# Performance work log

Measured on AMD Instinct MI355X. Metric: run time of the kernel, lower is better.

Reference implementation:

```python
import jax, jax.numpy as jnp
import numpy as np

B, S, D, H = 4, 2048, 768, 12
HD = D // H  # head_dim = 64


def setup_inputs() -> dict:
    key = jax.random.key(0)
    ks = jax.random.split(key, 5)
    scale = 0.02
    return {
        "x": jax.random.normal(ks[0], (B, S, D), dtype=jnp.float32),
        "wq": jax.random.normal(ks[1], (D, D), dtype=jnp.float32) * scale,
        "wk": jax.random.normal(ks[2], (D, D), dtype=jnp.float32) * scale,
        "wv": jax.random.normal(ks[3], (D, D), dtype=jnp.float32) * scale,
        "wo": jax.random.normal(ks[4], (D, D), dtype=jnp.float32) * scale,
        "bo": jnp.zeros((D,), dtype=jnp.float32),
    }


def reference(x, wq, wk, wv, wo, bo):
    b, s, d = x.shape
    # torch Linear: y = x @ W.T ; qkv_bias=False
    q = (x @ wq.T).reshape(b, s, H, HD).transpose(0, 2, 1, 3)  # [b,h,s,hd]
    k = (x @ wk.T).reshape(b, s, H, HD).transpose(0, 2, 1, 3)
    v = (x @ wv.T).reshape(b, s, H, HD).transpose(0, 2, 1, 3)
    scores = jnp.einsum("bhqd,bhkd->bhqk", q, k)  # full [b,h,s,s] score matrix
    causal = jnp.triu(jnp.ones((s, s), dtype=bool), k=1)
    scores = jnp.where(causal, -jnp.inf, scores)
    attn = jax.nn.softmax(scores / jnp.sqrt(jnp.float32(HD)), axis=-1)
    ctx = jnp.einsum("bhqk,bhkd->bhqd", attn, v)
    ctx = ctx.transpose(0, 2, 1, 3).reshape(b, s, d)
    return ctx @ wo.T + bo  # dropout is identity in eval mode
```

## Files before the change

kernel.cpp:

```cpp
#include <hip/hip_runtime.h>

#define H 12
#define S 2048
#define D 768
#define HD 64
#define BATCH 4
#define M_TOT (BATCH * S)

typedef __attribute__((ext_vector_type(8))) short bf16x8;
typedef __attribute__((ext_vector_type(4))) short bf16x4;
typedef __attribute__((ext_vector_type(4))) float f32x4;

__device__ __forceinline__ f32x4 mfma16(bf16x4 a, bf16x4 b, f32x4 c) {
#if defined(__HIP_DEVICE_COMPILE__)
#if __has_builtin(__builtin_amdgcn_mfma_f32_16x16x16bf16_1k)
  return __builtin_amdgcn_mfma_f32_16x16x16bf16_1k(a, b, c, 0, 0, 0);
#else
  asm volatile("v_mfma_f32_16x16x16_bf16 %0, %1, %2, %0"
               : "+v"(c) : "v"(a), "v"(b));
  return c;
#endif
#else
  (void)a; (void)b;
  return c;
#endif
}

__device__ __forceinline__ ushort f2bf(float f) {
  unsigned int x = __float_as_uint(f);
  x += 0x7fffu + ((x >> 16) & 1u);
  return (ushort)(x >> 16);
}

__device__ __forceinline__ uint cvt_pk_bf16(float lo, float hi) {
  uint r;
  asm("v_cvt_pk_bf16_f32 %0, %1, %2" : "=v"(r) : "v"(lo), "v"(hi));
  return r;
}

__device__ __forceinline__ void gload_lds16(const void* gsrc, void* lds) {
  __builtin_amdgcn_global_load_lds(
      (const __attribute__((address_space(1))) unsigned int*)gsrc,
      (__attribute__((address_space(3))) unsigned int*)lds, 16, 0, 0);
}

__global__ __launch_bounds__(256) void cast_all(
    const float* __restrict__ x, const float* __restrict__ wq,
    const float* __restrict__ wk, const float* __restrict__ wv,
    const float* __restrict__ wo, ushort* __restrict__ xb,
    ushort* __restrict__ wqb, ushort* __restrict__ wkb,
    ushort* __restrict__ wvb, ushort* __restrict__ wob) {
  const int NX = M_TOT * D / 4;
  const int NW = D * D / 4;
  int i = blockIdx.x * 256 + threadIdx.x;
  const float* src; ushort* dst; int off;
  if (i < NX) { src = x; dst = xb; off = i; }
  else {
    int j = i - NX; int w = j / NW; off = j - w * NW;
    src = (w == 0) ? wq : (w == 1) ? wk : (w == 2) ? wv : wo;
    dst = (w == 0) ? wqb : (w == 1) ? wkb : (w == 2) ? wvb : wob;
  }
  float4 f = reinterpret_cast<const float4*>(src)[off];
  ushort4 u;
  u.x = f2bf(f.x); u.y = f2bf(f.y); u.z = f2bf(f.z); u.w = f2bf(f.w);
  reinterpret_cast<ushort4*>(dst)[off] = u;
}

__global__ __launch_bounds__(256) void gemm_qkv(
    const ushort* __restrict__ xb, const ushort* __restrict__ wqb,
    const ushort* __restrict__ wkb, const ushort* __restrict__ wvb,
    ushort* __restrict__ qb, ushort* __restrict__ kb_,
    ushort* __restrict__ vtb, float qscale) {
  __shared__ ushort SM[2][8192];
  const int tid = threadIdx.x;
  const int lane = tid & 63, wid = tid >> 6;
  const int g = lane >> 4, li = lane & 15;
  const int wm = wid >> 1, wn = wid & 1;

  const int wg = blockIdx.x;
  const ushort *Ap, *Wp; ushort* ob; float osc; int m0, n0; bool vt;
  if (wg < 768) {
    vt = false;
    m0 = (wg & 63) * 128;
    const int y = wg >> 6;
    n0 = (y % 6) * 128;
    Ap = xb;
    if (y < 6) { Wp = wqb; ob = qb; osc = qscale; }
    else       { Wp = wkb; ob = kb_; osc = 1.0f; }
  } else {
    vt = true;
    const int t2 = wg - 768;
    m0 = (t2 % 6) * 128;
    n0 = (t2 / 6) * 128;
    Ap = wvb; Wp = xb; ob = vtb; osc = 1.0f;
  }

  const int rsub = lane >> 2;
  const int coff = (((lane & 3) ^ ((rsub >> 1) & 3)) << 3);

  auto stage = [&](int buf, int k0) {
#pragma unroll
    for (int rnd = 0; rnd < 2; ++rnd) {
      const int row0 = rnd * 64 + wid * 16;
      gload_lds16(&Ap[(size_t)(m0 + row0 + rsub) * 768 + k0 + coff], &SM[buf][row0 * 32]);
      gload_lds16(&Wp[(size_t)(n0 + row0 + rsub) * 768 + k0 + coff],
                  &SM[buf][4096 + row0 * 32]);
    }
  };

  f32x4 acc[4][4] = {};
  stage(0, 0);

  for (int kt = 0; kt < 24; ++kt) {
    const int cur = kt & 1;
    asm volatile("s_waitcnt vmcnt(0)" ::: "memory");
    __syncthreads();
    if (kt + 1 < 24) stage(cur ^ 1, (kt + 1) * 32);

    bf16x8 a[4], b[4];
#pragma unroll
    for (int i = 0; i < 4; ++i) {
      const int row = wm * 64 + i * 16 + li;
      a[i] = *reinterpret_cast<const bf16x8*>(
          &SM[cur][row * 32 + ((g ^ ((row >> 1) & 3)) << 3)]);
    }
#pragma unroll
    for (int j = 0; j < 4; ++j) {
      const int row = wn * 64 + j * 16 + li;
      b[j] = *reinterpret_cast<const bf16x8*>(
          &SM[cur][4096 + row * 32 + ((g ^ ((row >> 1) & 3)) << 3)]);
    }
    __builtin_amdgcn_s_setprio(1);
#pragma unroll
    for (int i = 0; i < 4; ++i)
#pragma unroll
      for (int j = 0; j < 4; ++j)
        acc[i][j] = __builtin_amdgcn_mfma_f32_16x16x32_bf16(a[i], b[j], acc[i][j], 0, 0, 0);
    __builtin_amdgcn_s_setprio(0);
  }

  __syncthreads();
  ushort* Cs = &SM[0][0];
#pragma unroll
  for (int i = 0; i < 4; ++i)
#pragma unroll
    for (int j = 0; j < 4; ++j)
#pragma unroll
      for (int r = 0; r < 4; ++r) {
        const int row = wm * 64 + i * 16 + g * 4 + r;
        const int col = wn * 64 + j * 16 + li;
        const int pc = ((((col >> 3) ^ (row & 7)) << 3) | (col & 7));
        Cs[row * 128 + pc] = f2bf(acc[i][j][r] * osc);
      }
  __syncthreads();

  const int row = tid >> 1, half = tid & 1;
  ushort* dst;
  if (!vt) {
    const int m = m0 + row;
    const int b_ = m >> 11, s_ = m & 2047;
    const int h_ = (n0 >> 6) + half;
    dst = &ob[(((size_t)b_ * H + h_) * S + s_) * HD];
  } else {
    const int mf = m0 + row;
    const int b_ = n0 >> 11;
    const int h_ = mf >> 6, hd_ = mf & 63;
    dst = &ob[(((size_t)b_ * H + h_) * HD + hd_) * S + (n0 & 2047) + half * 64];
  }
#pragma unroll
  for (int c8 = 0; c8 < 8; ++c8) {
    const int col = half * 64 + c8 * 8;
    const int chunk = (col >> 3) ^ (row & 7);
    bf16x8 vv = *reinterpret_cast<const bf16x8*>(&Cs[row * 128 + chunk * 8]);
    *reinterpret_cast<bf16x8*>(&dst[c8 * 8]) = vv;
  }
}

__global__ __launch_bounds__(256) void gemm_wo(const ushort* __restrict__ A,
                                               const ushort* __restrict__ W,
                                               float* __restrict__ out_f,
                                               const float* __restrict__ bias) {
  __shared__ ushort SM[2][8192];
  const int tid = threadIdx.x;
  const int lane = tid & 63, wid = tid >> 6;
  const int g = lane >> 4, li = lane & 15;
  const int wm = wid >> 1, wn = wid & 1;
  const int m0 = blockIdx.x * 128, n0 = blockIdx.y * 128;

  const int rsub = lane >> 2;
  const int coff = (((lane & 3) ^ ((rsub >> 1) & 3)) << 3);

  auto stage = [&](int buf, int k0) {
#pragma unroll
    for (int rnd = 0; rnd < 2; ++rnd) {
      const int row0 = rnd * 64 + wid * 16;
      gload_lds16(&A[(size_t)(m0 + row0 + rsub) * 768 + k0 + coff], &SM[buf][row0 * 32]);
      gload_lds16(&W[(size_t)(n0 + row0 + rsub) * 768 + k0 + coff],
                  &SM[buf][4096 + row0 * 32]);
    }
  };

  f32x4 acc[4][4] = {};
  stage(0, 0);

  for (int kt = 0; kt < 24; ++kt) {
    const int cur = kt & 1;
    asm volatile("s_waitcnt vmcnt(0)" ::: "memory");
    __syncthreads();
    if (kt + 1 < 24) stage(cur ^ 1, (kt + 1) * 32);

    bf16x8 a[4], b[4];
#pragma unroll
    for (int i = 0; i < 4; ++i) {
      const int row = wm * 64 + i * 16 + li;
      a[i] = *reinterpret_cast<const bf16x8*>(
          &SM[cur][row * 32 + ((g ^ ((row >> 1) & 3)) << 3)]);
    }
#pragma unroll
    for (int j = 0; j < 4; ++j) {
      const int row = wn * 64 + j * 16 + li;
      b[j] = *reinterpret_cast<const bf16x8*>(
          &SM[cur][4096 + row * 32 + ((g ^ ((row >> 1) & 3)) << 3)]);
    }
    __builtin_amdgcn_s_setprio(1);
#pragma unroll
    for (int i = 0; i < 4; ++i)
#pragma unroll
      for (int j = 0; j < 4; ++j)
        acc[i][j] = __builtin_amdgcn_mfma_f32_16x16x32_bf16(a[i], b[j], acc[i][j], 0, 0, 0);
    __builtin_amdgcn_s_setprio(0);
  }

#pragma unroll
  for (int i = 0; i < 4; ++i)
#pragma unroll
    for (int j = 0; j < 4; ++j)
#pragma unroll
      for (int r = 0; r < 4; ++r) {
        const int m = m0 + wm * 64 + i * 16 + g * 4 + r;
        const int n = n0 + wn * 64 + j * 16 + li;
        out_f[(size_t)m * 768 + n] = acc[i][j][r] + bias[n];
      }
}

__global__ __launch_bounds__(256) void attn_kernel(const ushort* __restrict__ Q,
                                                   const ushort* __restrict__ K,
                                                   const ushort* __restrict__ VT,
                                                   ushort* __restrict__ ctx) {
  __shared__ ushort Ks[2][64 * 64];
  __shared__ ushort Vts[2][64 * 64];

  const int tid = threadIdx.x;
  const int lane = tid & 63, wid = tid >> 6;
  const int g = lane >> 4, li = lane & 15;

  const int wg = blockIdx.x;
  const int xcd = wg & 7, t = wg >> 3;
  const int bh = xcd + 8 * (t >> 4);
  const int p = t & 15;
  const int qL = 64 * (31 - p), qS = 64 * p;

  const size_t base = (size_t)bh * S * HD;
  const size_t vtbase = (size_t)bh * HD * S;

  bf16x8 aq[2][2];
#pragma unroll
  for (int f = 0; f < 2; ++f) {
    const size_t qr = base + (size_t)((f ? qS : qL) + wid * 16 + li) * HD;
#pragma unroll
    for (int c = 0; c < 2; ++c)
      aq[f][c] = *reinterpret_cast<const bf16x8*>(&Q[qr + c * 32 + g * 8]);
  }

  f32x4 acc[2][4] = {};
  float lpart[2] = {0.f, 0.f};

  const int nkt = 32 - p;

  const int rsub = lane >> 3;
  const int c8e = (((lane & 7) ^ rsub) << 3);

  auto stage = [&](int buf, int k0) {
#pragma unroll
    for (int rnd = 0; rnd < 2; ++rnd) {
      const int row0 = rnd * 32 + wid * 8;
      gload_lds16(&K[base + (size_t)(k0 + row0 + rsub) * HD + c8e], &Ks[buf][row0 << 6]);
      gload_lds16(&VT[vtbase + (size_t)(row0 + rsub) * S + k0 + c8e], &Vts[buf][row0 << 6]);
    }
  };

  stage(0, 0);

  for (int kt = 0; kt < nkt; ++kt) {
    const int cur = kt & 1;
    const int k0 = kt * 64;
    const bool doS = (kt <= p);

    asm volatile("s_waitcnt vmcnt(0)" ::: "memory");
    __syncthreads();
    if (kt + 1 < nkt) stage(cur ^ 1, k0 + 64);

    f32x4 sc[2][4];
    __builtin_amdgcn_s_setprio(1);
#pragma unroll
    for (int ct = 0; ct < 4; ++ct) {
      const int row = ct * 16 + li, r7 = row & 7;
      const ushort* kr = &Ks[cur][row << 6];
      bf16x8 kb0 = *reinterpret_cast<const bf16x8*>(&kr[(g ^ r7) << 3]);
      bf16x8 kb1 = *reinterpret_cast<const bf16x8*>(&kr[((4 + g) ^ r7) << 3]);
      {
        f32x4 z = {};
        z = __builtin_amdgcn_mfma_f32_16x16x32_bf16(kb0, aq[0][0], z, 0, 0, 0);
        z = __builtin_amdgcn_mfma_f32_16x16x32_bf16(kb1, aq[0][1], z, 0, 0, 0);
        sc[0][ct] = z;
      }
      if (doS) {
        f32x4 z = {};
        z = __builtin_amdgcn_mfma_f32_16x16x32_bf16(kb0, aq[1][0], z, 0, 0, 0);
        z = __builtin_amdgcn_mfma_f32_16x16x32_bf16(kb1, aq[1][1], z, 0, 0, 0);
        sc[1][ct] = z;
      }
    }
    __builtin_amdgcn_s_setprio(0);

    if (kt == nkt - 1) {
      const int q = qL + wid * 16 + li;
#pragma unroll
      for (int ct = 0; ct < 4; ++ct)
#pragma unroll
        for (int r = 0; r < 4; ++r)
          if (k0 + ct * 16 + 4 * g + r > q) sc[0][ct][r] = -1e30f;
    }
    if (kt == p) {
      const int q = qS + wid * 16 + li;
#pragma unroll
      for (int ct = 0; ct < 4; ++ct)
#pragma unroll
        for (int r = 0; r < 4; ++r)
          if (k0 + ct * 16 + 4 * g + r > q) sc[1][ct][r] = -1e30f;
    }

    uint2 pf[2][4];
#pragma unroll
    for (int f = 0; f < 2; ++f) {
      if (f == 1 && !doS) break;
#pragma unroll
      for (int ct = 0; ct < 4; ++ct) {
        float p0 = __builtin_amdgcn_exp2f(sc[f][ct][0]);
        float p1 = __builtin_amdgcn_exp2f(sc[f][ct][1]);
        float p2 = __builtin_amdgcn_exp2f(sc[f][ct][2]);
        float p3 = __builtin_amdgcn_exp2f(sc[f][ct][3]);
        lpart[f] += (p0 + p1) + (p2 + p3);
        pf[f][ct].x = cvt_pk_bf16(p0, p1);
        pf[f][ct].y = cvt_pk_bf16(p2, p3);
      }
    }

    __builtin_amdgcn_s_setprio(1);
#pragma unroll
    for (int dt = 0; dt < 4; ++dt) {
      const int row = dt * 16 + li, r7 = row & 7;
      const ushort* vr = &Vts[cur][row << 6];
#pragma unroll
      for (int ct = 0; ct < 4; ++ct) {
        const int e = 16 * ct + 4 * g;
        const int phys = (((e >> 3) ^ r7) << 3) + (e & 7);
        bf16x4 vb = *reinterpret_cast<const bf16x4*>(&vr[phys]);
        acc[0][dt] = mfma16(*reinterpret_cast<const bf16x4*>(&pf[0][ct]), vb, acc[0][dt]);
        if (doS)
          acc[1][dt] = mfma16(*reinterpret_cast<const bf16x4*>(&pf[1][ct]), vb, acc[1][dt]);
      }
    }
    __builtin_amdgcn_s_setprio(0);
  }

  const int b = bh / H, h = bh % H;
#pragma unroll
  for (int f = 0; f < 2; ++f) {
    float l = lpart[f];
    l += __shfl_xor(l, 16);
    l += __shfl_xor(l, 32);
#pragma unroll
    for (int r = 0; r < 4; ++r) {
      float inv = 1.0f / __shfl(l, 4 * g + r);
      const int s = (f ? qS : qL) + wid * 16 + 4 * g + r;
#pragma unroll
      for (int dt = 0; dt < 4; ++dt)
        ctx[((size_t)(b * S + s)) * D + h * HD + dt * 16 + li] =
            f2bf(acc[f][dt][r] * inv);
    }
  }
}

extern "C" void kernel_launch(void* const* d_in, const int* in_sizes, int n_in,
                              void* d_out, int out_size, void* d_ws, size_t ws_size,
                              hipStream_t stream) {
  (void)in_sizes; (void)n_in; (void)out_size; (void)ws_size;
  const float* x  = (const float*)d_in[0];
  const float* wq = (const float*)d_in[1];
  const float* wk = (const float*)d_in[2];
  const float* wv = (const float*)d_in[3];
  const float* wo = (const float*)d_in[4];
  const float* bo = (const float*)d_in[5];
  float* out = (float*)d_out;

  const size_t xn = (size_t)M_TOT * D;
  const size_t wn = (size_t)D * D;

  ushort* p = (ushort*)d_ws;
  ushort* x_bf  = p; p += xn;
  ushort* wq_bf = p; p += wn;
  ushort* wk_bf = p; p += wn;
  ushort* wv_bf = p; p += wn;
  ushort* wo_bf = p; p += wn;
  ushort* q_bf  = p; p += xn;
  ushort* k_bf  = p; p += xn;
  ushort* vt_bf = p; p += xn;
  ushort* ctx_bf = x_bf;

  cast_all<<<8448, 256, 0, stream>>>(x, wq, wk, wv, wo,
                                     x_bf, wq_bf, wk_bf, wv_bf, wo_bf);

  const float QSCALE = 0.125f * 1.44269504f;
  gemm_qkv<<<1152, 256, 0, stream>>>(x_bf, wq_bf, wk_bf, wv_bf,
                                     q_bf, k_bf, vt_bf, QSCALE);

  attn_kernel<<<768, 256, 0, stream>>>(q_bf, k_bf, vt_bf, ctx_bf);

  gemm_wo<<<dim3(64, 6), 256, 0, stream>>>(ctx_bf, wo_bf, out, bo);
}
```

Baseline: 140.9 us.

## Use 16x16x32 MFMA for PV via LDS P relayout; shrink Wo GEMM M-tile

In attention, the bf16 probabilities are written to a per-wave LDS scratch and read back in the 8-element operand layout. This lets the PV product use the 16x16x32 bf16 MFMA with 128-bit V reads, replacing twice as many 16x16x16 MFMAs with 64-bit reads. Separately, the output-projection GEMM tile drops from 128 to 64 rows, doubling the grid to 768 blocks for better CU fill. The attention change adds LDS round-trip traffic and may need wave-level ordering between the P writes and reads; the smaller GEMM tile lowers data reuse per block.

```diff
diff --git a/kernel.cpp b/kernel.cpp
--- a/kernel.cpp
+++ b/kernel.cpp
@@ -8,23 +8,7 @@
 #define M_TOT (BATCH * S)
 
 typedef __attribute__((ext_vector_type(8))) short bf16x8;
-typedef __attribute__((ext_vector_type(4))) short bf16x4;
 typedef __attribute__((ext_vector_type(4))) float f32x4;
-
-__device__ __forceinline__ f32x4 mfma16(bf16x4 a, bf16x4 b, f32x4 c) {
-#if defined(__HIP_DEVICE_COMPILE__)
-#if __has_builtin(__builtin_amdgcn_mfma_f32_16x16x16bf16_1k)
-  return __builtin_amdgcn_mfma_f32_16x16x16bf16_1k(a, b, c, 0, 0, 0);
-#else
-  asm volatile("v_mfma_f32_16x16x16_bf16 %0, %1, %2, %0"
-               : "+v"(c) : "v"(a), "v"(b));
-  return c;
-#endif
-#else
-  (void)a; (void)b;
-  return c;
-#endif
-}
 
 __device__ __forceinline__ ushort f2bf(float f) {
   unsigned int x = __float_as_uint(f);
@@ -180,27 +164,28 @@
                                                const ushort* __restrict__ W,
                                                float* __restrict__ out_f,
                                                const float* __restrict__ bias) {
-  __shared__ ushort SM[2][8192];
+  __shared__ ushort SM[2][6144];
   const int tid = threadIdx.x;
   const int lane = tid & 63, wid = tid >> 6;
   const int g = lane >> 4, li = lane & 15;
   const int wm = wid >> 1, wn = wid & 1;
-  const int m0 = blockIdx.x * 128, n0 = blockIdx.y * 128;
+  const int m0 = blockIdx.x * 64, n0 = blockIdx.y * 128;
 
   const int rsub = lane >> 2;
   const int coff = (((lane & 3) ^ ((rsub >> 1) & 3)) << 3);
 
   auto stage = [&](int buf, int k0) {
+    gload_lds16(&A[(size_t)(m0 + wid * 16 + rsub) * 768 + k0 + coff],
+                &SM[buf][wid * 16 * 32]);
 #pragma unroll
     for (int rnd = 0; rnd < 2; ++rnd) {
       const int row0 = rnd * 64 + wid * 16;
-      gload_lds16(&A[(size_t)(m0 + row0 + rsub) * 768 + k0 + coff], &SM[buf][row0 * 32]);
       gload_lds16(&W[(size_t)(n0 + row0 + rsub) * 768 + k0 + coff],
-                  &SM[buf][4096 + row0 * 32]);
+                  &SM[buf][2048 + row0 * 32]);
     }
   };
 
-  f32x4 acc[4][4] = {};
+  f32x4 acc[2][4] = {};
   stage(0, 0);
 
   for (int kt = 0; kt < 24; ++kt) {
@@ -209,10 +194,10 @@
     __syncthreads();
     if (kt + 1 < 24) stage(cur ^ 1, (kt + 1) * 32);
 
-    bf16x8 a[4], b[4];
-#pragma unroll
-    for (int i = 0; i < 4; ++i) {
-      const int row = wm * 64 + i * 16 + li;
+    bf16x8 a[2], b[4];
+#pragma unroll
+    for (int i = 0; i < 2; ++i) {
+      const int row = wm * 32 + i * 16 + li;
       a[i] = *reinterpret_cast<const bf16x8*>(
           &SM[cur][row * 32 + ((g ^ ((row >> 1) & 3)) << 3)]);
     }
@@ -220,11 +205,11 @@
     for (int j = 0; j < 4; ++j) {
       const int row = wn * 64 + j * 16 + li;
       b[j] = *reinterpret_cast<const bf16x8*>(
-          &SM[cur][4096 + row * 32 + ((g ^ ((row >> 1) & 3)) << 3)]);
+          &SM[cur][2048 + row * 32 + ((g ^ ((row >> 1) & 3)) << 3)]);
     }
     __builtin_amdgcn_s_setprio(1);
 #pragma unroll
-    for (int i = 0; i < 4; ++i)
+    for (int i = 0; i < 2; ++i)
 #pragma unroll
       for (int j = 0; j < 4; ++j)
         acc[i][j] = __builtin_amdgcn_mfma_f32_16x16x32_bf16(a[i], b[j], acc[i][j], 0, 0, 0);
@@ -232,12 +217,12 @@
   }
 
 #pragma unroll
-  for (int i = 0; i < 4; ++i)
+  for (int i = 0; i < 2; ++i)
 #pragma unroll
     for (int j = 0; j < 4; ++j)
 #pragma unroll
       for (int r = 0; r < 4; ++r) {
-        const int m = m0 + wm * 64 + i * 16 + g * 4 + r;
+        const int m = m0 + wm * 32 + i * 16 + g * 4 + r;
         const int n = n0 + wn * 64 + j * 16 + li;
         out_f[(size_t)m * 768 + n] = acc[i][j][r] + bias[n];
       }
@@ -249,6 +234,7 @@
                                                    ushort* __restrict__ ctx) {
   __shared__ ushort Ks[2][64 * 64];
   __shared__ ushort Vts[2][64 * 64];
+  __shared__ ushort Ps[4][32][72];
 
   const int tid = threadIdx.x;
   const int lane = tid & 63, wid = tid >> 6;
@@ -340,7 +326,6 @@
           if (k0 + ct * 16 + 4 * g + r > q) sc[1][ct][r] = -1e30f;
     }
 
-    uint2 pf[2][4];
 #pragma unroll
     for (int f = 0; f < 2; ++f) {
       if (f == 1 && !doS) break;
@@ -351,24 +336,32 @@
         float p2 = __builtin_amdgcn_exp2f(sc[f][ct][2]);
         float p3 = __builtin_amdgcn_exp2f(sc[f][ct][3]);
         lpart[f] += (p0 + p1) + (p2 + p3);
-        pf[f][ct].x = cvt_pk_bf16(p0, p1);
-        pf[f][ct].y = cvt_pk_bf16(p2, p3);
-      }
-    }
-
+        uint2 pw;
+        pw.x = cvt_pk_bf16(p0, p1);
+        pw.y = cvt_pk_bf16(p2, p3);
+        *reinterpret_cast<uint2*>(&Ps[wid][f * 16 + li][ct * 16 + 4 * g]) = pw;
+      }
+    }
+
+    bf16x8 pa[2][2];
+    pa[0][0] = *reinterpret_cast<const bf16x8*>(&Ps[wid][li][g * 8]);
+    pa[0][1] = *reinterpret_cast<const bf16x8*>(&Ps[wid][li][32 + g * 8]);
+    if (doS) {
+      pa[1][0] = *reinterpret_cast<const bf16x8*>(&Ps[wid][16 + li][g * 8]);
+      pa[1][1] = *reinterpret_cast<const bf16x8*>(&Ps[wid][16 + li][32 + g * 8]);
+    }
     __builtin_amdgcn_s_setprio(1);
 #pragma unroll
     for (int dt = 0; dt < 4; ++dt) {
       const int row = dt * 16 + li, r7 = row & 7;
       const ushort* vr = &Vts[cur][row << 6];
-#pragma unroll
-      for (int ct = 0; ct < 4; ++ct) {
-        const int e = 16 * ct + 4 * g;
-        const int phys = (((e >> 3) ^ r7) << 3) + (e & 7);
-        bf16x4 vb = *reinterpret_cast<const bf16x4*>(&vr[phys]);
-        acc[0][dt] = mfma16(*reinterpret_cast<const bf16x4*>(&pf[0][ct]), vb, acc[0][dt]);
-        if (doS)
-          acc[1][dt] = mfma16(*reinterpret_cast<const bf16x4*>(&pf[1][ct]), vb, acc[1][dt]);
+      bf16x8 vb0 = *reinterpret_cast<const bf16x8*>(&vr[(g ^ r7) << 3]);
+      bf16x8 vb1 = *reinterpret_cast<const bf16x8*>(&vr[((4 + g) ^ r7) << 3]);
+      acc[0][dt] = __builtin_amdgcn_mfma_f32_16x16x32_bf16(pa[0][0], vb0, acc[0][dt], 0, 0, 0);
+      acc[0][dt] = __builtin_amdgcn_mfma_f32_16x16x32_bf16(pa[0][1], vb1, acc[0][dt], 0, 0, 0);
+      if (doS) {
+        acc[1][dt] = __builtin_amdgcn_mfma_f32_16x16x32_bf16(pa[1][0], vb0, acc[1][dt], 0, 0, 0);
+        acc[1][dt] = __builtin_amdgcn_mfma_f32_16x16x32_bf16(pa[1][1], vb1, acc[1][dt], 0, 0, 0);
       }
     }
     __builtin_amdgcn_s_setprio(0);
@@ -427,5 +420,5 @@
 
   attn_kernel<<<768, 256, 0, stream>>>(q_bf, k_bf, vt_bf, ctx_bf);
 
-  gemm_wo<<<dim3(64, 6), 256, 0, stream>>>(ctx_bf, wo_bf, out, bo);
-}
+  gemm_wo<<<dim3(128, 6), 256, 0, stream>>>(ctx_bf, wo_bf, out, bo);
+}
```

Result: faster. 135.4 us (-3.9%).
